# Performance work log

Measured on AMD Instinct MI355X. Metric: run time of the kernel, lower is better.

Reference implementation:

```python
import jax, jax.numpy as jnp
import numpy as np

HIDDEN = 2048
NUM_Q_HEADS = 32
NUM_KV_HEADS = 8
HEAD_DIM = HIDDEN // NUM_Q_HEADS          # 64
GROUP = NUM_Q_HEADS // NUM_KV_HEADS       # 4
B, L = 2, 2048


def setup_inputs() -> dict:
    key = jax.random.key(0)
    ks = jax.random.split(key, 10)
    s = 1.0 / np.sqrt(HIDDEN)
    return {
        "x": jax.random.normal(ks[0], (B, L, HIDDEN), dtype=jnp.float32),
        "attention_mask": jnp.ones((B, L), dtype=jnp.int32),
        "q_w": jax.random.uniform(ks[1], (NUM_Q_HEADS * HEAD_DIM, HIDDEN), jnp.float32, -s, s),
        "q_b": jax.random.uniform(ks[2], (NUM_Q_HEADS * HEAD_DIM,), jnp.float32, -s, s),
        "k_w": jax.random.uniform(ks[3], (NUM_KV_HEADS * HEAD_DIM, HIDDEN), jnp.float32, -s, s),
        "k_b": jax.random.uniform(ks[4], (NUM_KV_HEADS * HEAD_DIM,), jnp.float32, -s, s),
        "v_w": jax.random.uniform(ks[5], (NUM_KV_HEADS * HEAD_DIM, HIDDEN), jnp.float32, -s, s),
        "v_b": jax.random.uniform(ks[6], (NUM_KV_HEADS * HEAD_DIM,), jnp.float32, -s, s),
        "o_w": jax.random.uniform(ks[7], (HIDDEN, HIDDEN), jnp.float32, -s, s),
        "o_b": jax.random.uniform(ks[8], (HIDDEN,), jnp.float32, -s, s),
    }


def reference(x, attention_mask, q_w, q_b, k_w, k_b, v_w, v_b, o_w, o_b):
    Bsz, Ls, _ = x.shape
    # projections (torch Linear: x @ W^T + b)
    q = x @ q_w.T + q_b                      # [B, L, Hq*D]
    k = x @ k_w.T + k_b                      # [B, L, Hkv*D]
    v = x @ v_w.T + v_b                      # [B, L, Hkv*D]
    # grouped reshape: q head h = kv*GROUP + g, matching repeat_interleave on k/v
    q = q.reshape(Bsz, Ls, NUM_KV_HEADS, GROUP, HEAD_DIM)
    k = k.reshape(Bsz, Ls, NUM_KV_HEADS, HEAD_DIM)
    v = v.reshape(Bsz, Ls, NUM_KV_HEADS, HEAD_DIM)
    scale = 1.0 / np.sqrt(HEAD_DIM).astype(np.float32)
    # scores: [B, Hkv, G, Lq, Lk]
    scores = jnp.einsum('bqhgd,bkhd->bhgqk', q, k) * scale
    neg = jnp.finfo(scores.dtype).min
    # causal mask
    causal = jnp.triu(jnp.ones((Ls, Ls), dtype=bool), k=1)
    scores = jnp.where(causal, neg, scores)
    # key padding mask: attention_mask==0 -> masked
    pad = (attention_mask == 0)[:, None, None, None, :]  # [B,1,1,1,Lk]
    scores = jnp.where(pad, neg, scores)
    attn = jax.nn.softmax(scores, axis=-1)
    # dropout is identity in eval / p=0
    out = jnp.einsum('bhgqk,bkhd->bqhgd', attn, v)
    out = out.reshape(Bsz, Ls, HIDDEN)
    return out @ o_w.T + o_b
```

## Files before the change

kernel.cpp:

```cpp
#include <hip/hip_runtime.h>
#include <hip/hip_bf16.h>

typedef __attribute__((ext_vector_type(8))) short s16x8;
typedef __attribute__((ext_vector_type(4))) short s16x4;
typedef __attribute__((ext_vector_type(2))) short s16x2;
typedef __attribute__((ext_vector_type(4))) float f32x4;
typedef __attribute__((ext_vector_type(4))) unsigned int u32x4;

#define L_ 2048
#define HID 2048
#define DH 64

__device__ __forceinline__ short f2bs(float f) {
    __hip_bfloat16 h = __float2bfloat16(f);
    return *reinterpret_cast<short*>(&h);
}
__device__ __forceinline__ unsigned int pkbf(float a, float b) {
    return (unsigned int)(unsigned short)f2bs(a) |
           ((unsigned int)(unsigned short)f2bs(b) << 16);
}
__device__ __forceinline__ float bpermf(int byteidx, float v) {
    int r = __builtin_amdgcn_ds_bpermute(byteidx, __builtin_bit_cast(int, v));
    return __builtin_bit_cast(float, r);
}
__device__ __forceinline__ s16x4 load4_bf16(const float* p) {
    const float4 v = *(const float4*)p;
    s16x4 r; r.x = f2bs(v.x); r.y = f2bs(v.y); r.z = f2bs(v.z); r.w = f2bs(v.w);
    return r;
}
__device__ __forceinline__ s16x4 load4_bf16(const __hip_bfloat16* p) {
    return *(const s16x4*)p;
}
__device__ __forceinline__ void store1(float* p, float v) { *p = v; }
__device__ __forceinline__ void store1(__hip_bfloat16* p, float v) { *p = __float2bfloat16(v); }

__device__ __forceinline__ void glds16(const __hip_bfloat16* g, __hip_bfloat16* l) {
    __builtin_amdgcn_global_load_lds(
        (const __attribute__((address_space(1))) unsigned int*)g,
        (__attribute__((address_space(3))) unsigned int*)l, 16, 0, 0);
}

__global__ __launch_bounds__(256) void cvt8(const float* __restrict__ in,
                                            __hip_bfloat16* __restrict__ out, int n8) {
    const int i = blockIdx.x * 256 + threadIdx.x;
    if (i >= n8) return;
    const float4* p = (const float4*)in + (long)i * 2;
    const float4 a = p[0], b = p[1];
    s16x8 r;
    r[0] = f2bs(a.x); r[1] = f2bs(a.y); r[2] = f2bs(a.z); r[3] = f2bs(a.w);
    r[4] = f2bs(b.x); r[5] = f2bs(b.y); r[6] = f2bs(b.z); r[7] = f2bs(b.w);
    *((s16x8*)out + i) = r;
}

__global__ __launch_bounds__(256) void gemm_qkv(
    const __hip_bfloat16* __restrict__ A,
    const __hip_bfloat16* __restrict__ W,
    const float* __restrict__ qb, const float* __restrict__ kb2,
    const float* __restrict__ vb2,
    __hip_bfloat16* __restrict__ Qb, __hip_bfloat16* __restrict__ Kt,
    __hip_bfloat16* __restrict__ Vt)
{
    const int K = 2048;
    __shared__ __hip_bfloat16 sA[128*32];
    __shared__ __hip_bfloat16 sB[128*32];
    const int tid  = threadIdx.x;
    const int wid  = tid >> 6;
    const int lane = tid & 63;
    const int m0 = blockIdx.x * 128;
    const int n0 = blockIdx.y * 128;
    const int wm = (wid >> 1) * 64;
    const int wn = (wid & 1) * 64;

    f32x4 acc[4][4];
#pragma unroll
    for (int i = 0; i < 4; ++i)
#pragma unroll
        for (int j = 0; j < 4; ++j)
#pragma unroll
            for (int r = 0; r < 4; ++r) acc[i][j][r] = 0.0f;

    const int sr = tid >> 2;
    const int sc = (tid & 3) * 8;
    const __hip_bfloat16* gA = A + (long)(m0 + sr) * K + sc;
    const __hip_bfloat16* gB = W + (long)(n0 + sr) * K + sc;
    __hip_bfloat16* lA = &sA[sr*32 + sc];
    __hip_bfloat16* lB = &sB[sr*32 + sc];

    const int arow0 = wm + (lane & 15);
    const int brow0 = wn + (lane & 15);
    const int koff  = (lane >> 4) * 8;

    for (int kt = 0; kt < 64; ++kt) {
        glds16(gA,              lA);
        glds16(gA + (long)64*K, lA + 64*32);
        glds16(gB,              lB);
        glds16(gB + (long)64*K, lB + 64*32);
        gA += 32; gB += 32;
        __syncthreads();

        s16x8 af[4], bfr[4];
#pragma unroll
        for (int mi = 0; mi < 4; ++mi)
            af[mi] = *(const s16x8*)&sA[(arow0 + mi*16)*32 + koff];
#pragma unroll
        for (int ni = 0; ni < 4; ++ni)
            bfr[ni] = *(const s16x8*)&sB[(brow0 + ni*16)*32 + koff];
#pragma unroll
        for (int mi = 0; mi < 4; ++mi)
#pragma unroll
            for (int ni = 0; ni < 4; ++ni)
                acc[mi][ni] = __builtin_amdgcn_mfma_f32_16x16x32_bf16(
                    af[mi], bfr[ni], acc[mi][ni], 0, 0, 0);
        __syncthreads();
    }

    __hip_bfloat16* C; int ldc, coff; const float* bias;
    if (n0 < 2048)      { C = Qb; ldc = 2048; coff = n0;        bias = qb  + n0; }
    else if (n0 < 2560) { C = Kt; ldc = 512;  coff = n0 - 2048; bias = kb2 + (n0 - 2048); }
    else                { C = Vt; ldc = 512;  coff = n0 - 2560; bias = vb2 + (n0 - 2560); }

    float bvals[4];
#pragma unroll
    for (int ni = 0; ni < 4; ++ni)
        bvals[ni] = bias[wn + ni*16 + (lane & 15)];
#pragma unroll
    for (int mi = 0; mi < 4; ++mi) {
        const int row = m0 + wm + mi*16 + (lane >> 4)*4;
#pragma unroll
        for (int ni = 0; ni < 4; ++ni) {
            const int col = coff + wn + ni*16 + (lane & 15);
#pragma unroll
            for (int r = 0; r < 4; ++r)
                C[(long)(row + r)*ldc + col] = __float2bfloat16(acc[mi][ni][r] + bvals[ni]);
        }
    }
}

template <typename TC>
__global__ __launch_bounds__(256) void gemm_fast(
    const __hip_bfloat16* __restrict__ A,
    const __hip_bfloat16* __restrict__ Bw,
    const float* __restrict__ bias,
    TC* __restrict__ C, int M, int N, int K)
{
    __shared__ __hip_bfloat16 sA[128*32];
    __shared__ __hip_bfloat16 sB[128*32];
    const int tid  = threadIdx.x;
    const int wid  = tid >> 6;
    const int lane = tid & 63;
    const int m0 = blockIdx.x * 128;
    const int n0 = blockIdx.y * 128;
    const int wm = (wid >> 1) * 64;
    const int wn = (wid & 1) * 64;

    f32x4 acc[4][4];
#pragma unroll
    for (int i = 0; i < 4; ++i)
#pragma unroll
        for (int j = 0; j < 4; ++j)
#pragma unroll
            for (int r = 0; r < 4; ++r) acc[i][j][r] = 0.0f;

    const int sr = tid >> 2;
    const int sc = (tid & 3) * 8;
    const __hip_bfloat16* gA = A  + (long)(m0 + sr) * K + sc;
    const __hip_bfloat16* gB = Bw + (long)(n0 + sr) * K + sc;
    __hip_bfloat16* lA = &sA[sr*32 + sc];
    __hip_bfloat16* lB = &sB[sr*32 + sc];

    const int arow0 = wm + (lane & 15);
    const int brow0 = wn + (lane & 15);
    const int koff  = (lane >> 4) * 8;

    const int nk = K >> 5;
    for (int kt = 0; kt < nk; ++kt) {
        glds16(gA,              lA);
        glds16(gA + (long)64*K, lA + 64*32);
        glds16(gB,              lB);
        glds16(gB + (long)64*K, lB + 64*32);
        gA += 32; gB += 32;
        __syncthreads();

        s16x8 af[4], bfr[4];
#pragma unroll
        for (int mi = 0; mi < 4; ++mi)
            af[mi] = *(const s16x8*)&sA[(arow0 + mi*16)*32 + koff];
#pragma unroll
        for (int ni = 0; ni < 4; ++ni)
            bfr[ni] = *(const s16x8*)&sB[(brow0 + ni*16)*32 + koff];
#pragma unroll
        for (int mi = 0; mi < 4; ++mi)
#pragma unroll
            for (int ni = 0; ni < 4; ++ni)
                acc[mi][ni] = __builtin_amdgcn_mfma_f32_16x16x32_bf16(
                    af[mi], bfr[ni], acc[mi][ni], 0, 0, 0);
        __syncthreads();
    }

    float bvals[4];
#pragma unroll
    for (int ni = 0; ni < 4; ++ni)
        bvals[ni] = bias[n0 + wn + ni*16 + (lane & 15)];
#pragma unroll
    for (int mi = 0; mi < 4; ++mi) {
        const int row = m0 + wm + mi*16 + (lane >> 4)*4;
#pragma unroll
        for (int ni = 0; ni < 4; ++ni) {
            const int col = n0 + wn + ni*16 + (lane & 15);
#pragma unroll
            for (int r = 0; r < 4; ++r)
                store1(&C[(long)(row + r)*N + col], acc[mi][ni][r] + bvals[ni]);
        }
    }
}

template <typename TA, typename TC>
__global__ __launch_bounds__(256) void gemm_bt_bias(
    const TA* __restrict__ A, const float* __restrict__ Bw,
    const float* __restrict__ bias, TC* __restrict__ C,
    int M, int N, int K)
{
    __shared__ __hip_bfloat16 sA[128*32];
    __shared__ __hip_bfloat16 sB[128*32];
    const int tid  = threadIdx.x;
    const int wid  = tid >> 6;
    const int lane = tid & 63;
    const int m0 = blockIdx.x * 128;
    const int n0 = blockIdx.y * 128;
    const int wm = (wid >> 1) * 64;
    const int wn = (wid & 1) * 64;

    f32x4 acc[4][4];
#pragma unroll
    for (int i = 0; i < 4; ++i)
#pragma unroll
        for (int j = 0; j < 4; ++j)
#pragma unroll
            for (int r = 0; r < 4; ++r) acc[i][j][r] = 0.0f;

    const int sr = tid >> 3;
    const int sc = (tid & 7) * 4;
    const TA*    gA = A  + (long)(m0 + sr) * K + sc;
    const float* gB = Bw + (long)(n0 + sr) * K + sc;

    const int arow0 = wm + (lane & 15);
    const int brow0 = wn + (lane & 15);
    const int koff  = (lane >> 4) * 8;

    const int nk = K >> 5;
    for (int kt = 0; kt < nk; ++kt) {
        s16x4 a0 = load4_bf16(gA);
        s16x4 a1 = load4_bf16(gA + (long)32*K);
        s16x4 a2 = load4_bf16(gA + (long)64*K);
        s16x4 a3 = load4_bf16(gA + (long)96*K);
        s16x4 b0 = load4_bf16(gB);
        s16x4 b1 = load4_bf16(gB + (long)32*K);
        s16x4 b2 = load4_bf16(gB + (long)64*K);
        s16x4 b3 = load4_bf16(gB + (long)96*K);
        gA += 32; gB += 32;
        *(s16x4*)&sA[(sr     )*32 + sc] = a0;
        *(s16x4*)&sA[(sr + 32)*32 + sc] = a1;
        *(s16x4*)&sA[(sr + 64)*32 + sc] = a2;
        *(s16x4*)&sA[(sr + 96)*32 + sc] = a3;
        *(s16x4*)&sB[(sr     )*32 + sc] = b0;
        *(s16x4*)&sB[(sr + 32)*32 + sc] = b1;
        *(s16x4*)&sB[(sr + 64)*32 + sc] = b2;
        *(s16x4*)&sB[(sr + 96)*32 + sc] = b3;
        __syncthreads();

        s16x8 af[4], bfr[4];
#pragma unroll
        for (int mi = 0; mi < 4; ++mi)
            af[mi] = *(const s16x8*)&sA[(arow0 + mi*16)*32 + koff];
#pragma unroll
        for (int ni = 0; ni < 4; ++ni)
            bfr[ni] = *(const s16x8*)&sB[(brow0 + ni*16)*32 + koff];
#pragma unroll
        for (int mi = 0; mi < 4; ++mi)
#pragma unroll
            for (int ni = 0; ni < 4; ++ni)
                acc[mi][ni] = __builtin_amdgcn_mfma_f32_16x16x32_bf16(
                    af[mi], bfr[ni], acc[mi][ni], 0, 0, 0);
        __syncthreads();
    }

    float bvals[4];
#pragma unroll
    for (int ni = 0; ni < 4; ++ni)
        bvals[ni] = bias[n0 + wn + ni*16 + (lane & 15)];
#pragma unroll
    for (int mi = 0; mi < 4; ++mi) {
        const int row = m0 + wm + mi*16 + (lane >> 4)*4;
#pragma unroll
        for (int ni = 0; ni < 4; ++ni) {
            const int col = n0 + wn + ni*16 + (lane & 15);
#pragma unroll
            for (int r = 0; r < 4; ++r)
                store1(&C[(long)(row + r)*N + col], acc[mi][ni][r] + bvals[ni]);
        }
    }
}

#define LDK 72
#define LDV 72

__global__ __launch_bounds__(512, 6) void gqa_flash(
    const __hip_bfloat16* __restrict__ Q,
    const __hip_bfloat16* __restrict__ Kb,
    const __hip_bfloat16* __restrict__ Vb,
    const int* __restrict__ amask,
    __hip_bfloat16* __restrict__ O)
{
    __shared__ __hip_bfloat16 sK[2][64*LDK];
    __shared__ __hip_bfloat16 sVt[2][64*LDV];
    __shared__ unsigned int sPp[8][512];

    const int tid  = threadIdx.x;
    const int wid  = tid >> 6;
    const int lane = tid & 63;
    const int bx = blockIdx.x;
    const int bh = blockIdx.y;
    const int b  = bh >> 5;
    const int h  = bh & 31;
    const int kv = h >> 2;

    const __hip_bfloat16* Kg = Kb + (long)(b*L_)*512 + kv*DH;
    const __hip_bfloat16* Vg = Vb + (long)(b*L_)*512 + kv*DH;
    const int* mg = amask + b*L_;

    const int lcol = lane & 15;
    const int g    = lane >> 4;

    const int kr = tid >> 3;
    const int kc = (tid & 7) * 8;
    const int vj = (tid & 31) * 2;
    const int vd = (tid >> 5) * 4;
    const int qsr = tid >> 2;
    const int qsc = (tid & 3) * 16;

    unsigned int* myP = sPp[wid];
    const float c1 = 0.18033688011112042f;

    for (int ph = 0; ph < 2; ++ph) {
        const int qt = ph ? (15 - bx) : bx;
        const int jmax = 2*qt + 1;
        const __hip_bfloat16* Qg = Q + (long)(b*L_ + qt*128)*HID + h*DH;

        __syncthreads();
        {
            s16x8 q0 = *(const s16x8*)(Qg + (long)qsr*HID + qsc);
            s16x8 q1 = *(const s16x8*)(Qg + (long)qsr*HID + qsc + 8);
            __hip_bfloat16* dst = (qsr < 64) ? &sK[0][qsr*LDK + qsc]
                                             : &sK[1][(qsr-64)*LDK + qsc];
            *(s16x8*)&dst[0] = q0;
            *(s16x8*)&dst[8] = q1;
        }
        __syncthreads();
        s16x8 qf[2];
        {
            const __hip_bfloat16* qbuf = (wid < 4)
                ? &sK[0][((wid & 3)*16 + lcol)*LDK]
                : &sK[1][((wid & 3)*16 + lcol)*LDK];
            qf[0] = *(const s16x8*)&qbuf[g*8];
            qf[1] = *(const s16x8*)&qbuf[32 + g*8];
        }
        __syncthreads();

        {
            s16x8 k0 = *(const s16x8*)(Kg + (long)kr*512 + kc);
            *(s16x8*)&sK[0][kr*LDK + kc] = k0;
            s16x4 v0 = *(const s16x4*)(Vg + (long)vj*512 + vd);
            s16x4 v1 = *(const s16x4*)(Vg + (long)(vj+1)*512 + vd);
            short* sv = (short*)sVt[0];
#pragma unroll
            for (int i = 0; i < 4; ++i) {
                s16x2 pr; pr.x = v0[i]; pr.y = v1[i];
                *(s16x2*)&sv[(vd+i)*LDV + vj] = pr;
            }
        }

        float mrun = -30000.0f, lrl = 0.0f;
        f32x4 oacc[4];
#pragma unroll
        for (int nt = 0; nt < 4; ++nt)
#pragma unroll
            for (int r = 0; r < 4; ++r) oacc[nt][r] = 0.0f;

        for (int jt = 0; jt <= jmax; ++jt) {
            const int cur = jt & 1;
            __syncthreads();

            const int jn = (jt < jmax) ? jt + 1 : jt;
            s16x8 kreg = *(const s16x8*)(Kg + (long)(jn*64 + kr)*512 + kc);
            s16x4 v0r  = *(const s16x4*)(Vg + (long)(jn*64 + vj)*512 + vd);
            s16x4 v1r  = *(const s16x4*)(Vg + (long)(jn*64 + vj + 1)*512 + vd);
            const int mv = mg[jt*64 + lane];
            const unsigned long long bal = __ballot(mv == 0);

            f32x4 sacc[4];
#pragma unroll
            for (int ct = 0; ct < 4; ++ct)
#pragma unroll
                for (int r = 0; r < 4; ++r) sacc[ct][r] = 0.0f;
#pragma unroll
            for (int ks = 0; ks < 2; ++ks)
#pragma unroll
                for (int ct = 0; ct < 4; ++ct) {
                    s16x8 kf = *(const s16x8*)&sK[cur][(ct*16 + lcol)*LDK + ks*32 + g*8];
                    sacc[ct] = __builtin_amdgcn_mfma_f32_16x16x32_bf16(
                        kf, qf[ks], sacc[ct], 0, 0, 0);
                }

            if (bal) {
#pragma unroll
                for (int ct = 0; ct < 4; ++ct) {
                    const unsigned nib = (unsigned)(bal >> (ct*16 + g*4)) & 15u;
#pragma unroll
                    for (int r = 0; r < 4; ++r)
                        if (nib & (1u << r)) sacc[ct][r] = -2.0e5f;
                }
            }
            if (jt >= 2*qt) {
                const int qrow = qt*128 + wid*16 + lcol;
#pragma unroll
                for (int ct = 0; ct < 4; ++ct) {
                    const int jb = jt*64 + ct*16 + g*4;
#pragma unroll
                    for (int r = 0; r < 4; ++r)
                        if (jb + r > qrow) sacc[ct][r] = -2.0e5f;
                }
            }

            float mx = sacc[0][0];
#pragma unroll
            for (int ct = 0; ct < 4; ++ct)
#pragma unroll
                for (int r = 0; r < 4; ++r) mx = fmaxf(mx, sacc[ct][r]);
            mx = fmaxf(mx, __shfl_xor(mx, 16));
            mx = fmaxf(mx, __shfl_xor(mx, 32));
            const float mn = fmaxf(mrun, mx * c1);
            const float al = exp2f(mrun - mn);
            mrun = mn;

            float ps = 0.0f;
            unsigned int pk[4][2];
#pragma unroll
            for (int ct = 0; ct < 4; ++ct) {
                const float p0 = exp2f(fmaf(sacc[ct][0], c1, -mn));
                const float p1 = exp2f(fmaf(sacc[ct][1], c1, -mn));
                const float p2 = exp2f(fmaf(sacc[ct][2], c1, -mn));
                const float p3 = exp2f(fmaf(sacc[ct][3], c1, -mn));
                ps += (p0 + p1) + (p2 + p3);
                pk[ct][0] = pkbf(p0, p1);
                pk[ct][1] = pkbf(p2, p3);
            }
            lrl = lrl * al + ps;

#pragma unroll
            for (int ct = 0; ct < 4; ++ct) {
                const int xb = (ct & 1) << 4;
                myP[ct*128 +      ((g*16 + lcol) ^ xb)] = pk[ct][0];
                myP[ct*128 + 64 + ((g*16 + lcol) ^ xb)] = pk[ct][1];
            }

            float alr[4];
#pragma unroll
            for (int r = 0; r < 4; ++r)
                alr[r] = bpermf((g*4 + r) << 2, al);
#pragma unroll
            for (int nt = 0; nt < 4; ++nt)
#pragma unroll
                for (int r = 0; r < 4; ++r) oacc[nt][r] *= alr[r];

            if (jt < jmax) {
                const int nb = cur ^ 1;
                *(s16x8*)&sK[nb][kr*LDK + kc] = kreg;
                short* sv = (short*)sVt[nb];
#pragma unroll
                for (int i = 0; i < 4; ++i) {
                    s16x2 pr; pr.x = v0r[i]; pr.y = v1r[i];
                    *(s16x2*)&sv[(vd+i)*LDV + vj] = pr;
                }
            }

#pragma unroll
            for (int ks = 0; ks < 2; ++ks) {
                const int ct = ks*2 + (g >> 1);
                const int xb = (ct & 1) << 4;
                const int w0 = (2*g) & 3;
                const int w1 = (2*g + 1) & 3;
                u32x4 pu;
                pu.x = myP[ct*128 +      ((w0*16 + lcol) ^ xb)];
                pu.y = myP[ct*128 + 64 + ((w0*16 + lcol) ^ xb)];
                pu.z = myP[ct*128 +      ((w1*16 + lcol) ^ xb)];
                pu.w = myP[ct*128 + 64 + ((w1*16 + lcol) ^ xb)];
                const s16x8 pf = __builtin_bit_cast(s16x8, pu);
#pragma unroll
                for (int nt = 0; nt < 4; ++nt) {
                    s16x8 vf = *(const s16x8*)&sVt[cur][(nt*16 + lcol)*LDV + ks*32 + g*8];
                    oacc[nt] = __builtin_amdgcn_mfma_f32_16x16x32_bf16(
                        pf, vf, oacc[nt], 0, 0, 0);
                }
            }
        }

        lrl += __shfl_xor(lrl, 16);
        lrl += __shfl_xor(lrl, 32);
        const float inv = 1.0f / lrl;
        float invr[4];
#pragma unroll
        for (int r = 0; r < 4; ++r)
            invr[r] = bpermf((g*4 + r) << 2, inv);

        __hip_bfloat16* Og = O + (long)(b*L_ + qt*128)*HID + h*DH;
#pragma unroll
        for (int r = 0; r < 4; ++r) {
            const int row = wid*16 + g*4 + r;
#pragma unroll
            for (int nt = 0; nt < 4; ++nt)
                Og[(long)row*HID + nt*16 + lcol] =
                    __float2bfloat16(oacc[nt][r] * invr[r]);
        }
    }
}

extern "C" void kernel_launch(void* const* d_in, const int* in_sizes, int n_in,
                              void* d_out, int out_size, void* d_ws, size_t ws_size,
                              hipStream_t stream) {
    const float* x   = (const float*)d_in[0];
    const int*   am  = (const int*)d_in[1];
    const float* q_w = (const float*)d_in[2];
    const float* q_b = (const float*)d_in[3];
    const float* k_w = (const float*)d_in[4];
    const float* k_b = (const float*)d_in[5];
    const float* v_w = (const float*)d_in[6];
    const float* v_b = (const float*)d_in[7];
    const float* o_w = (const float*)d_in[8];
    const float* o_b = (const float*)d_in[9];
    float* out = (float*)d_out;
    char* ws = (char*)d_ws;
    dim3 blk(256);

    if (ws_size >= 37748736) {
        __hip_bfloat16* Qb   = (__hip_bfloat16*)d_out;
        __hip_bfloat16* xb   = (__hip_bfloat16*)((char*)d_out + 16777216);
        __hip_bfloat16* wcat = (__hip_bfloat16*)(ws);
        __hip_bfloat16* qwb  = (__hip_bfloat16*)(ws);
        __hip_bfloat16* kwb  = (__hip_bfloat16*)(ws + 8388608);
        __hip_bfloat16* vwb  = (__hip_bfloat16*)(ws + 10485760);
        __hip_bfloat16* Kt   = (__hip_bfloat16*)(ws + 12582912);
        __hip_bfloat16* Vt   = (__hip_bfloat16*)(ws + 16777216);
        __hip_bfloat16* Ob   = (__hip_bfloat16*)(ws + 20971520);
        __hip_bfloat16* owb  = qwb;

        cvt8<<<4096, blk, 0, stream>>>(x,   xb,  1048576);
        cvt8<<<2048, blk, 0, stream>>>(q_w, qwb, 524288);
        cvt8<<< 512, blk, 0, stream>>>(k_w, kwb, 131072);
        cvt8<<< 512, blk, 0, stream>>>(v_w, vwb, 131072);
        gemm_qkv<<<dim3(32, 24), blk, 0, stream>>>(xb, wcat, q_b, k_b, v_b, Qb, Kt, Vt);
        cvt8<<<2048, blk, 0, stream>>>(o_w, owb, 524288);
        gqa_flash<<<dim3(8, 64), dim3(512), 0, stream>>>(Qb, Kt, Vt, am, Ob);
        gemm_fast<float><<<dim3(32, 16), blk, 0, stream>>>(Ob, owb, o_b, out, 4096, 2048, 2048);
    } else {
        __hip_bfloat16* Qb = (__hip_bfloat16*)d_out;
        __hip_bfloat16* Kt = (__hip_bfloat16*)(ws);
        __hip_bfloat16* Vt = (__hip_bfloat16*)(ws + 4194304);
        __hip_bfloat16* Ob = (__hip_bfloat16*)(ws + 8388608);
        gemm_bt_bias<float, __hip_bfloat16><<<dim3(32,16), blk, 0, stream>>>(x, q_w, q_b, Qb, 4096, 2048, 2048);
        gemm_bt_bias<float, __hip_bfloat16><<<dim3(32, 4), blk, 0, stream>>>(x, k_w, k_b, Kt, 4096,  512, 2048);
        gemm_bt_bias<float, __hip_bfloat16><<<dim3(32, 4), blk, 0, stream>>>(x, v_w, v_b, Vt, 4096,  512, 2048);
        gqa_flash<<<dim3(8, 64), dim3(512), 0, stream>>>(Qb, Kt, Vt, am, Ob);
        gemm_bt_bias<__hip_bfloat16, float><<<dim3(32,16), blk, 0, stream>>>(Ob, o_w, o_b, out, 4096, 2048, 2048);
    }
}
```

Before: 349.9 us.

## Fuse input conversions, speed up P packing, skip unneeded rescale in flash loop

Merges the four fp32→bf16 conversion launches into a single kernel. In the flash attention loop it also packs P with a cheaper round-half-up bit trick, writes P to LDS inline, and skips the output-accumulator rescale when no lane's running max changed. The prefetch no longer clamps the next tile index, so the last iteration now reads one tile past jmax. That read can go out of bounds, and the half-up rounding differs slightly from round-to-nearest-even.

```diff
diff --git a/kernel.cpp b/kernel.cpp
--- a/kernel.cpp
+++ b/kernel.cpp
@@ -15,9 +15,10 @@
     __hip_bfloat16 h = __float2bfloat16(f);
     return *reinterpret_cast<short*>(&h);
 }
-__device__ __forceinline__ unsigned int pkbf(float a, float b) {
-    return (unsigned int)(unsigned short)f2bs(a) |
-           ((unsigned int)(unsigned short)f2bs(b) << 16);
+__device__ __forceinline__ unsigned int pkbf_fast(float a, float b) {
+    unsigned ua = __builtin_bit_cast(unsigned, a) + 0x8000u;
+    unsigned ub = __builtin_bit_cast(unsigned, b) + 0x8000u;
+    return __builtin_amdgcn_perm(ub, ua, 0x07060302u);
 }
 __device__ __forceinline__ float bpermf(int byteidx, float v) {
     int r = __builtin_amdgcn_ds_bpermute(byteidx, __builtin_bit_cast(int, v));
@@ -40,16 +41,35 @@
         (__attribute__((address_space(3))) unsigned int*)l, 16, 0, 0);
 }
 
+__device__ __forceinline__ void cvt8_body(const float* src, __hip_bfloat16* dst, long i) {
+    const float4* p = (const float4*)src + i * 2;
+    const float4 a = p[0], b = p[1];
+    s16x8 r;
+    r[0] = f2bs(a.x); r[1] = f2bs(a.y); r[2] = f2bs(a.z); r[3] = f2bs(a.w);
+    r[4] = f2bs(b.x); r[5] = f2bs(b.y); r[6] = f2bs(b.z); r[7] = f2bs(b.w);
+    *((s16x8*)dst + i) = r;
+}
+
+__global__ __launch_bounds__(256) void cvt_xqkv(
+    const float* __restrict__ x,  const float* __restrict__ qw,
+    const float* __restrict__ kw, const float* __restrict__ vw,
+    __hip_bfloat16* __restrict__ xb,  __hip_bfloat16* __restrict__ qwb,
+    __hip_bfloat16* __restrict__ kwb, __hip_bfloat16* __restrict__ vwb)
+{
+    long i = (long)blockIdx.x * 256 + threadIdx.x;
+    const float* src; __hip_bfloat16* dst;
+    if (i < 1048576)      { src = x;  dst = xb;  }
+    else if (i < 1572864) { src = qw; dst = qwb; i -= 1048576; }
+    else if (i < 1703936) { src = kw; dst = kwb; i -= 1572864; }
+    else                  { src = vw; dst = vwb; i -= 1703936; }
+    cvt8_body(src, dst, i);
+}
+
 __global__ __launch_bounds__(256) void cvt8(const float* __restrict__ in,
                                             __hip_bfloat16* __restrict__ out, int n8) {
     const int i = blockIdx.x * 256 + threadIdx.x;
     if (i >= n8) return;
-    const float4* p = (const float4*)in + (long)i * 2;
-    const float4 a = p[0], b = p[1];
-    s16x8 r;
-    r[0] = f2bs(a.x); r[1] = f2bs(a.y); r[2] = f2bs(a.z); r[3] = f2bs(a.w);
-    r[4] = f2bs(b.x); r[5] = f2bs(b.y); r[6] = f2bs(b.z); r[7] = f2bs(b.w);
-    *((s16x8*)out + i) = r;
+    cvt8_body(in, out, i);
 }
 
 __global__ __launch_bounds__(256) void gemm_qkv(
@@ -390,10 +410,10 @@
             const int cur = jt & 1;
             __syncthreads();
 
-            const int jn = (jt < jmax) ? jt + 1 : jt;
-            s16x8 kreg = *(const s16x8*)(Kg + (long)(jn*64 + kr)*512 + kc);
-            s16x4 v0r  = *(const s16x4*)(Vg + (long)(jn*64 + vj)*512 + vd);
-            s16x4 v1r  = *(const s16x4*)(Vg + (long)(jn*64 + vj + 1)*512 + vd);
+            const long pno = (long)((jt + 1)*64) * 512;
+            s16x8 kreg = *(const s16x8*)(Kg + pno + (long)kr*512 + kc);
+            s16x4 v0r  = *(const s16x4*)(Vg + pno + (long)vj*512 + vd);
+            s16x4 v1r  = *(const s16x4*)(Vg + pno + (long)(vj+1)*512 + vd);
             const int mv = mg[jt*64 + lane];
             const unsigned long long bal = __ballot(mv == 0);
 
@@ -431,11 +451,11 @@
                 }
             }
 
-            float mx = sacc[0][0];
-#pragma unroll
-            for (int ct = 0; ct < 4; ++ct)
-#pragma unroll
-                for (int r = 0; r < 4; ++r) mx = fmaxf(mx, sacc[ct][r]);
+            float mxa = fmaxf(fmaxf(sacc[0][0], sacc[0][1]), fmaxf(sacc[0][2], sacc[0][3]));
+            float mxb = fmaxf(fmaxf(sacc[1][0], sacc[1][1]), fmaxf(sacc[1][2], sacc[1][3]));
+            float mxc = fmaxf(fmaxf(sacc[2][0], sacc[2][1]), fmaxf(sacc[2][2], sacc[2][3]));
+            float mxd = fmaxf(fmaxf(sacc[3][0], sacc[3][1]), fmaxf(sacc[3][2], sacc[3][3]));
+            float mx = fmaxf(fmaxf(mxa, mxb), fmaxf(mxc, mxd));
             mx = fmaxf(mx, __shfl_xor(mx, 16));
             mx = fmaxf(mx, __shfl_xor(mx, 32));
             const float mn = fmaxf(mrun, mx * c1);
@@ -443,7 +463,6 @@
             mrun = mn;
 
             float ps = 0.0f;
-            unsigned int pk[4][2];
 #pragma unroll
             for (int ct = 0; ct < 4; ++ct) {
                 const float p0 = exp2f(fmaf(sacc[ct][0], c1, -mn));
@@ -451,26 +470,22 @@
                 const float p2 = exp2f(fmaf(sacc[ct][2], c1, -mn));
                 const float p3 = exp2f(fmaf(sacc[ct][3], c1, -mn));
                 ps += (p0 + p1) + (p2 + p3);
-                pk[ct][0] = pkbf(p0, p1);
-                pk[ct][1] = pkbf(p2, p3);
+                const int xb = (ct & 1) << 4;
+                myP[ct*128 +      ((g*16 + lcol) ^ xb)] = pkbf_fast(p0, p1);
+                myP[ct*128 + 64 + ((g*16 + lcol) ^ xb)] = pkbf_fast(p2, p3);
             }
             lrl = lrl * al + ps;
 
-#pragma unroll
-            for (int ct = 0; ct < 4; ++ct) {
-                const int xb = (ct & 1) << 4;
-                myP[ct*128 +      ((g*16 + lcol) ^ xb)] = pk[ct][0];
-                myP[ct*128 + 64 + ((g*16 + lcol) ^ xb)] = pk[ct][1];
-            }
-
-            float alr[4];
-#pragma unroll
-            for (int r = 0; r < 4; ++r)
-                alr[r] = bpermf((g*4 + r) << 2, al);
-#pragma unroll
-            for (int nt = 0; nt < 4; ++nt)
-#pragma unroll
-                for (int r = 0; r < 4; ++r) oacc[nt][r] *= alr[r];
+            if (__any(al < 1.0f)) {
+                float alr[4];
+#pragma unroll
+                for (int r = 0; r < 4; ++r)
+                    alr[r] = bpermf((g*4 + r) << 2, al);
+#pragma unroll
+                for (int nt = 0; nt < 4; ++nt)
+#pragma unroll
+                    for (int r = 0; r < 4; ++r) oacc[nt][r] *= alr[r];
+            }
 
             if (jt < jmax) {
                 const int nb = cur ^ 1;
@@ -553,10 +568,7 @@
         __hip_bfloat16* Ob   = (__hip_bfloat16*)(ws + 20971520);
         __hip_bfloat16* owb  = qwb;
 
-        cvt8<<<4096, blk, 0, stream>>>(x,   xb,  1048576);
-        cvt8<<<2048, blk, 0, stream>>>(q_w, qwb, 524288);
-        cvt8<<< 512, blk, 0, stream>>>(k_w, kwb, 131072);
-        cvt8<<< 512, blk, 0, stream>>>(v_w, vwb, 131072);
+        cvt_xqkv<<<7168, blk, 0, stream>>>(x, q_w, k_w, v_w, xb, qwb, kwb, vwb);
         gemm_qkv<<<dim3(32, 24), blk, 0, stream>>>(xb, wcat, q_b, k_b, v_b, Qb, Kt, Vt);
         cvt8<<<2048, blk, 0, stream>>>(o_w, owb, 524288);
         gqa_flash<<<dim3(8, 64), dim3(512), 0, stream>>>(Qb, Kt, Vt, am, Ob);
```

Result: faster. 326.3 us (-6.7%).
